# Kernel tuning notes

Hardware: AMD Instinct MI355X
Metric: run time of the kernel (lower is better)

## Reference

```python
import jax, jax.numpy as jnp
import numpy as np

H = 16  # num_heads
NEG = -1.0e9


def setup_inputs() -> dict:
    key = jax.random.key(0)
    ks = jax.random.split(key, 12)
    B, Q, D, S = 2, 2048, 1024, 512
    sc = 0.02
    return {
        "main_input": jax.random.normal(ks[0], (B, Q, D), jnp.float32),
        "side_input": jax.random.normal(ks[1], (S, D), jnp.float32),
        "att_mask": jax.random.randint(ks[2], (B, Q, Q + S), 0, 2, jnp.int32),
        "Wq": jax.random.normal(ks[3], (D, D), jnp.float32) * sc,
        "bq": jnp.zeros((D,), jnp.float32),
        "Wk": jax.random.normal(ks[4], (D, D), jnp.float32) * sc,
        "bk": jnp.zeros((D,), jnp.float32),
        "Wv": jax.random.normal(ks[5], (D, D), jnp.float32) * sc,
        "bv": jnp.zeros((D,), jnp.float32),
        "Wo": jax.random.normal(ks[6], (D, D), jnp.float32) * sc,
        "bo": jnp.zeros((D,), jnp.float32),
    }


def _heads(x, W, b):
    # x: [..., D] -> [..., H, d]
    y = x @ W + b
    return y.reshape(y.shape[:-1] + (H, y.shape[-1] // H))


def reference(main_input, side_input, att_mask, Wq, bq, Wk, bk, Wv, bv, Wo, bo):
    B, Q, D = main_input.shape
    S = side_input.shape[0]
    d = D // H
    q = _heads(main_input, Wq, bq)          # [B,Q,H,d]
    k = _heads(main_input, Wk, bk)          # [B,Q,H,d]
    v = _heads(main_input, Wv, bv)          # [B,Q,H,d]
    sk = _heads(side_input, Wk, bk)         # [S,H,d] (shared projections)
    sv = _heads(side_input, Wv, bv)         # [S,H,d]
    scores_main = jnp.einsum('bqhd,bkhd->bhqk', q, k)
    scores_side = jnp.einsum('bqhd,khd->bhqk', q, sk)
    scores = jnp.concatenate([scores_main, scores_side], axis=3)  # [B,H,Q,Q+S]
    scores = scores / jnp.sqrt(jnp.asarray(d, scores.dtype))
    adder = NEG * (1.0 - att_mask.astype(scores.dtype))[:, None, :, :]
    probs = jax.nn.softmax(scores + adder, axis=-1)
    out_main = jnp.einsum('bhqk,bkhd->bqhd', probs[..., :Q], v)
    out_side = jnp.einsum('bhqk,khd->bqhd', probs[..., Q:], sv)
    att = (out_main + out_side).reshape(B, Q, D)
    return att @ Wo + bo
```

## Files before the change

### kernel.cpp

```cpp
#include <hip/hip_runtime.h>
#include <cstdint>

typedef short s16x8 __attribute__((ext_vector_type(8)));
typedef short s16x4 __attribute__((ext_vector_type(4)));
typedef unsigned short u16x4 __attribute__((ext_vector_type(4)));
typedef float f32x4 __attribute__((ext_vector_type(4)));
typedef float f32x16 __attribute__((ext_vector_type(16)));
typedef unsigned int u32x4 __attribute__((ext_vector_type(4)));

#define ND 1024
#define NH 16
#define DH 64
#define NQ 2048
#define NL 2560
#define MMAIN 4096
#define MCAT 4608
#define Q_SCALE 0.18033688011112042f

__device__ __forceinline__ unsigned short f2b(float f) {
  unsigned u = __builtin_bit_cast(unsigned, f);
  u += 0x7FFFu + ((u >> 16) & 1u);
  return (unsigned short)(u >> 16);
}

__device__ __forceinline__ void gload16(const void* g, void* l) {
  __builtin_amdgcn_global_load_lds(
      (const __attribute__((address_space(1))) void*)(unsigned long long)(uintptr_t)g,
      (__attribute__((address_space(3))) void*)(unsigned)(uintptr_t)l,
      16, 0, 0);
}

__device__ __forceinline__ f32x4 mfma16(s16x8 a, s16x8 b, f32x4 c) {
  return __builtin_amdgcn_mfma_f32_16x16x32_bf16(a, b, c, 0, 0, 0);
}
__device__ __forceinline__ f32x16 mfma32(s16x8 a, s16x8 b, f32x16 c) {
  return __builtin_amdgcn_mfma_f32_32x32x16_bf16(a, b, c, 0, 0, 0);
}

__device__ __forceinline__ float exp2g(float x) {
#if __has_builtin(__builtin_amdgcn_exp2f)
  return __builtin_amdgcn_exp2f(x);
#else
  return exp2f(x);
#endif
}

__device__ __forceinline__ int sext_bit(unsigned w, int c) {
#if __has_builtin(__builtin_amdgcn_sbfe)
  return __builtin_amdgcn_sbfe((int)w, c, 1);
#else
  return -(int)((w >> c) & 1u);
#endif
}

__device__ __forceinline__ unsigned cvt_pk_bf16(float lo, float hi) {
  unsigned d;
  asm("v_cvt_pk_bf16_f32 %0, %1, %2" : "=v"(d) : "v"(lo), "v"(hi));
  return d;
}

__device__ __forceinline__ void plane32_swap(unsigned& a, unsigned& b) {
  asm("v_permlane32_swap_b32 %0, %1" : "+v"(a), "+v"(b));
}

__device__ __forceinline__ f32x16 z16() {
  f32x16 v;
#pragma unroll
  for (int i = 0; i < 16; ++i) v[i] = 0.f;
  return v;
}


__global__ __launch_bounds__(256) void k_convert_x(const float* __restrict__ mainp,
                                                   const float* __restrict__ sidep,
                                                   short* __restrict__ xcat) {
  size_t i4 = ((size_t)blockIdx.x * 256 + threadIdx.x) * 4;
  const float* src = (i4 < (size_t)MMAIN * ND) ? (mainp + i4) : (sidep + (i4 - (size_t)MMAIN * ND));
  float4 v = *(const float4*)src;
  s16x4 o;
  o[0] = (short)f2b(v.x); o[1] = (short)f2b(v.y);
  o[2] = (short)f2b(v.z); o[3] = (short)f2b(v.w);
  *(s16x4*)(xcat + i4) = o;
}

__global__ __launch_bounds__(256) void k_transpose_w(const float* __restrict__ W0,
                                                     const float* __restrict__ W1,
                                                     const float* __restrict__ W2,
                                                     const float* __restrict__ W3,
                                                     short* __restrict__ Wt) {
  __shared__ float T[64][65];
  const float* W = blockIdx.z == 0 ? W0 : blockIdx.z == 1 ? W1 : blockIdx.z == 2 ? W2 : W3;
  short* out = Wt + (size_t)blockIdx.z * (ND * ND);
  const int tid = threadIdx.x;
  const int r = tid >> 2, c0 = (tid & 3) * 16;
  const int k0 = blockIdx.x * 64, n0 = blockIdx.y * 64;
#pragma unroll
  for (int i = 0; i < 4; ++i) {
    float4 v = *(const float4*)(W + (size_t)(k0 + r) * ND + n0 + c0 + i * 4);
    T[r][c0 + i * 4 + 0] = v.x; T[r][c0 + i * 4 + 1] = v.y;
    T[r][c0 + i * 4 + 2] = v.z; T[r][c0 + i * 4 + 3] = v.w;
  }
  __syncthreads();
  s16x8 o0, o1;
#pragma unroll
  for (int i = 0; i < 8; ++i) o0[i] = (short)f2b(T[c0 + i][r]);
#pragma unroll
  for (int i = 0; i < 8; ++i) o1[i] = (short)f2b(T[c0 + 8 + i][r]);
  *(s16x8*)(out + (size_t)(n0 + r) * ND + k0 + c0) = o0;
  *(s16x8*)(out + (size_t)(n0 + r) * ND + k0 + c0 + 8) = o1;
}

__global__ __launch_bounds__(256) void k_pack_mask(const int* __restrict__ mask,
                                                   unsigned* __restrict__ pm) {
  int W = blockIdx.x * 256 + threadIdx.x;
  const int4* src = (const int4*)(mask + (size_t)W * 32);
  unsigned bits = 0;
#pragma unroll
  for (int i = 0; i < 8; ++i) {
    int4 v = src[i];
    bits |= (unsigned)(v.x & 1) << (i * 4 + 0);
    bits |= (unsigned)(v.y & 1) << (i * 4 + 1);
    bits |= (unsigned)(v.z & 1) << (i * 4 + 2);
    bits |= (unsigned)(v.w & 1) << (i * 4 + 3);
  }
  pm[W] = bits;
}


__global__ __launch_bounds__(256) void k_gemm_qkv(const short* __restrict__ A,
                                                  const short* __restrict__ Bt,
                                                  const float* __restrict__ bqp,
                                                  const float* __restrict__ bkp,
                                                  const float* __restrict__ bvp,
                                                  short* __restrict__ qb,
                                                  short* __restrict__ kb,
                                                  short* __restrict__ vt) {
  __shared__ __align__(16) short As[128 * 64];
  __shared__ __align__(16) short Bs[128 * 64];
  const int tid = threadIdx.x;
  const int w = tid >> 6, l = tid & 63;
  const int lg = l >> 4, li = l & 15;
  const int wr = w >> 1, wc = w & 1;
  const int fid = blockIdx.x + 24 * blockIdx.y;
  const int rid = (fid & 7) * 108 + (fid >> 3);
  const int m0 = (rid / 24) * 128, n0 = (rid % 24) * 128;

  f32x4 acc[4][4];
#pragma unroll
  for (int i = 0; i < 4; ++i)
#pragma unroll
    for (int j = 0; j < 4; ++j) acc[i][j] = (f32x4){0.f, 0.f, 0.f, 0.f};

  const int cb = (l & 7) ^ (l >> 3);
  const int rsub = l >> 3;

  for (int kt = 0; kt < 16; ++kt) {
    __syncthreads();
#pragma unroll
    for (int i = 0; i < 4; ++i) {
      int c = w * 4 + i;
      int rr = c * 8 + rsub;
      gload16(A + (size_t)(m0 + rr) * ND + kt * 64 + cb * 8, As + c * 512);
      gload16(Bt + (size_t)(n0 + rr) * ND + kt * 64 + cb * 8, Bs + c * 512);
    }
    __syncthreads();
#pragma unroll
    for (int kk = 0; kk < 2; ++kk) {
      const int blk = (((kk * 4) + lg) ^ (l & 7)) * 8;
      s16x8 af[4], bf[4];
#pragma unroll
      for (int mf = 0; mf < 4; ++mf)
        af[mf] = *(const s16x8*)(As + (wr * 64 + mf * 16 + li) * 64 + blk);
#pragma unroll
      for (int nf = 0; nf < 4; ++nf)
        bf[nf] = *(const s16x8*)(Bs + (wc * 64 + nf * 16 + li) * 64 + blk);
#pragma unroll
      for (int mf = 0; mf < 4; ++mf)
#pragma unroll
        for (int nf = 0; nf < 4; ++nf)
          acc[mf][nf] = mfma16(af[mf], bf[nf], acc[mf][nf]);
    }
  }

#pragma unroll
  for (int mf = 0; mf < 4; ++mf) {
#pragma unroll
    for (int nf = 0; nf < 4; ++nf) {
      const int n = n0 + wc * 64 + nf * 16 + li;
      const int proj = n >> 10, nn = n & 1023;
      const int h = nn >> 6, dd = nn & 63;
      const float bn = (proj == 0 ? bqp : proj == 1 ? bkp : bvp)[nn];
      const int mbase = m0 + wr * 64 + mf * 16 + lg * 4;
      if (proj == 0) {
        if (mbase < MMAIN) {
#pragma unroll
          for (int r = 0; r < 4; ++r) {
            int m = mbase + r;
            int b = m >> 11, q = m & 2047;
            qb[((size_t)(b * NH + h) * NQ + q) * DH + dd] =
                (short)f2b((acc[mf][nf][r] + bn) * Q_SCALE);
          }
        }
      } else if (proj == 1) {
#pragma unroll
        for (int r = 0; r < 4; ++r) {
          int m = mbase + r;
          short v = (short)f2b(acc[mf][nf][r] + bn);
          if (m < MMAIN) {
            int b = m >> 11, p = m & 2047;
            kb[((size_t)(b * NH + h) * NL + p) * DH + dd] = v;
          } else {
            int p = NQ + (m - MMAIN);
            kb[((size_t)h * NL + p) * DH + dd] = v;
            kb[((size_t)(NH + h) * NL + p) * DH + dd] = v;
          }
        }
      } else {
        u16x4 vv;
#pragma unroll
        for (int r = 0; r < 4; ++r) vv[r] = f2b(acc[mf][nf][r] + bn);
        if (mbase < MMAIN) {
          int b = mbase >> 11, p = mbase & 2047;
          *(u16x4*)(vt + ((size_t)(b * NH + h) * DH + dd) * NL + p) = vv;
        } else {
          int p = NQ + (mbase - MMAIN);
          *(u16x4*)(vt + ((size_t)h * DH + dd) * NL + p) = vv;
          *(u16x4*)(vt + ((size_t)(NH + h) * DH + dd) * NL + p) = vv;
        }
      }
    }
  }
}


__global__ __launch_bounds__(256) void k_gemm_out(const short* __restrict__ A,
                                                  const short* __restrict__ Bt,
                                                  const float* __restrict__ bias,
                                                  float* __restrict__ outp) {
  __shared__ __align__(16) short As[128 * 64];
  __shared__ __align__(16) short Bs[128 * 64];
  const int tid = threadIdx.x;
  const int w = tid >> 6, l = tid & 63;
  const int lg = l >> 4, li = l & 15;
  const int wr = w >> 1, wc = w & 1;
  const int fid = blockIdx.x + 8 * blockIdx.y;
  const int rid = (fid & 7) * 32 + (fid >> 3);
  const int m0 = (rid / 8) * 128, n0 = (rid % 8) * 128;

  f32x4 acc[4][4];
#pragma unroll
  for (int i = 0; i < 4; ++i)
#pragma unroll
    for (int j = 0; j < 4; ++j) acc[i][j] = (f32x4){0.f, 0.f, 0.f, 0.f};

  const int cb = (l & 7) ^ (l >> 3);
  const int rsub = l >> 3;

  for (int kt = 0; kt < 16; ++kt) {
    __syncthreads();
#pragma unroll
    for (int i = 0; i < 4; ++i) {
      int c = w * 4 + i;
      int rr = c * 8 + rsub;
      gload16(A + (size_t)(m0 + rr) * ND + kt * 64 + cb * 8, As + c * 512);
      gload16(Bt + (size_t)(n0 + rr) * ND + kt * 64 + cb * 8, Bs + c * 512);
    }
    __syncthreads();
#pragma unroll
    for (int kk = 0; kk < 2; ++kk) {
      const int blk = (((kk * 4) + lg) ^ (l & 7)) * 8;
      s16x8 af[4], bf[4];
#pragma unroll
      for (int mf = 0; mf < 4; ++mf)
        af[mf] = *(const s16x8*)(As + (wr * 64 + mf * 16 + li) * 64 + blk);
#pragma unroll
      for (int nf = 0; nf < 4; ++nf)
        bf[nf] = *(const s16x8*)(Bs + (wc * 64 + nf * 16 + li) * 64 + blk);
#pragma unroll
      for (int mf = 0; mf < 4; ++mf)
#pragma unroll
        for (int nf = 0; nf < 4; ++nf)
          acc[mf][nf] = mfma16(af[mf], bf[nf], acc[mf][nf]);
    }
  }

#pragma unroll
  for (int mf = 0; mf < 4; ++mf) {
#pragma unroll
    for (int nf = 0; nf < 4; ++nf) {
      const int n = n0 + wc * 64 + nf * 16 + li;
      const float bn = bias[n];
      const int mbase = m0 + wr * 64 + mf * 16 + lg * 4;
#pragma unroll
      for (int r = 0; r < 4; ++r)
        outp[(size_t)(mbase + r) * ND + n] = acc[mf][nf][r] + bn;
    }
  }
}


#define PROC_TILE(STV, WSV, PB0, PB1)                                        \
  do {                                                                       \
    unsigned pk_[8];                                                         \
    _Pragma("unroll") for (int r_ = 0; r_ < 16; ++r_) {                      \
      const int c_ = (r_ & 3) + 8 * (r_ >> 2);                               \
      float p_ = exp2g(STV[r_]);                                             \
      STV[r_] = __builtin_bit_cast(                                          \
          float, __builtin_bit_cast(unsigned, p_) &                          \
                     (unsigned)sext_bit(WSV, c_));                           \
    }                                                                        \
    _Pragma("unroll") for (int m_ = 0; m_ < 8; ++m_)                         \
        pk_[m_] = cvt_pk_bf16(STV[2 * m_], STV[2 * m_ + 1]);                 \
    plane32_swap(pk_[0], pk_[2]);                                            \
    plane32_swap(pk_[1], pk_[3]);                                            \
    plane32_swap(pk_[4], pk_[6]);                                            \
    plane32_swap(pk_[5], pk_[7]);                                            \
    {                                                                        \
      u32x4 t_ = {pk_[0], pk_[1], pk_[2], pk_[3]};                           \
      PB0 = __builtin_bit_cast(s16x8, t_);                                   \
    }                                                                        \
    {                                                                        \
      u32x4 t_ = {pk_[4], pk_[5], pk_[6], pk_[7]};                           \
      PB1 = __builtin_bit_cast(s16x8, t_);                                   \
    }                                                                        \
  } while (0)

#define ATTN_TILE(CUR, T, DONEXT)                                            \
  do {                                                                       \
    uint2 mw_ = *(const uint2*)(pmrow + 2 * (T));                            \
    if (DONEXT) {                                                            \
      const int tn_ = (T) + 1;                                               \
      gload16(kg0 + (size_t)tn_ * 4096, klA + ((CUR) ^ 1) * 8192);           \
      gload16(kg1 + (size_t)tn_ * 4096, klB + ((CUR) ^ 1) * 8192);           \
      gload16(vg0 + tn_ * 64, vlA + ((CUR) ^ 1) * 8192);                     \
      gload16(vg1 + tn_ * 64, vlB + ((CUR) ^ 1) * 8192);                     \
    }                                                                        \
    f32x16 st0_, st1_;                                                       \
    __builtin_amdgcn_s_setprio(1);                                           \
    {                                                                        \
      s16x8 k0_ = *(const s16x8*)(ldsb + (CUR) * 8192 + koff[0]);            \
      s16x8 k1_ = *(const s16x8*)(ldsb + (CUR) * 8192 + koff[0] + 4096);     \
      st0_ = mfma32(k0_, qa[0], ZACC);                                       \
      st1_ = mfma32(k1_, qa[0], ZACC);                                       \
    }                                                                        \
    _Pragma("unroll") for (int ks_ = 1; ks_ < 4; ++ks_) {                    \
      s16x8 k0_ = *(const s16x8*)(ldsb + (CUR) * 8192 + koff[ks_]);          \
      s16x8 k1_ = *(const s16x8*)(ldsb + (CUR) * 8192 + koff[ks_] + 4096);   \
      st0_ = mfma32(k0_, qa[ks_], st0_);                                     \
      st1_ = mfma32(k1_, qa[ks_], st1_);                                     \
    }                                                                        \
    __builtin_amdgcn_s_setprio(0);                                           \
    unsigned ws0_ = mw_.x >> (hi * 4), ws1_ = mw_.y >> (hi * 4);             \
    s16x8 pbA_[4];                                                           \
    PROC_TILE(st0_, ws0_, pbA_[0], pbA_[1]);                                 \
    PROC_TILE(st1_, ws1_, pbA_[2], pbA_[3]);                                 \
    __builtin_amdgcn_s_setprio(1);                                           \
    _Pragma("unroll") for (int ks_ = 0; ks_ < 4; ++ks_) {                    \
      s16x8 v0_ = *(const s16x8*)(ldsb + 16384 + (CUR) * 8192 + koff[ks_]);  \
      s16x8 v1_ =                                                            \
          *(const s16x8*)(ldsb + 16384 + (CUR) * 8192 + koff[ks_] + 4096);   \
      ot0 = mfma32(v0_, pbA_[ks_], ot0);                                     \
      ot1 = mfma32(v1_, pbA_[ks_], ot1);                                     \
      lacc = mfma32(ones8, pbA_[ks_], lacc);                                 \
    }                                                                        \
    __builtin_amdgcn_s_setprio(0);                                           \
    __syncthreads();                                                         \
  } while (0)

__global__ __launch_bounds__(256) void k_attn2(const short* __restrict__ qbuf,
                                               const short* __restrict__ kbuf,
                                               const short* __restrict__ vtbuf,
                                               const unsigned* __restrict__ pmask,
                                               short* __restrict__ attbuf) {
  __shared__ __align__(16) short lds[16384];
  char* ldsb = (char*)lds;

  const int tid = threadIdx.x;
  const int w = tid >> 6, l = tid & 63;
  const int li = l & 31, hi = l >> 5;
  const int bh = blockIdx.x;
  const int b = bh >> 4, h = bh & 15;
  const int qr0 = blockIdx.y * 128 + w * 32;
  const size_t bhs = (size_t)bh;

  s16x8 qa[4];
  {
    const short* qp = qbuf + (bhs * NQ + qr0 + li) * DH + hi * 8;
#pragma unroll
    for (int ks = 0; ks < 4; ++ks) qa[ks] = *(const s16x8*)(qp + ks * 16);
  }

  int koff[4];
#pragma unroll
  for (int ks = 0; ks < 4; ++ks)
    koff[ks] = li * 128 + ((((ks << 1) | hi) ^ (li & 7)) << 4);

  const int crow = l >> 3;
  const int ccol = (l & 7) ^ crow;
  const short* kg0 = kbuf + (bhs * NL + (2 * w) * 8 + crow) * DH + ccol * 8;
  const short* kg1 = kbuf + (bhs * NL + (2 * w + 1) * 8 + crow) * DH + ccol * 8;
  const short* vg0 = vtbuf + (bhs * DH + (2 * w) * 8 + crow) * NL + ccol * 8;
  const short* vg1 = vtbuf + (bhs * DH + (2 * w + 1) * 8 + crow) * NL + ccol * 8;
  char* klA = ldsb + (2 * w) * 1024;
  char* klB = ldsb + (2 * w + 1) * 1024;
  char* vlA = ldsb + 16384 + (2 * w) * 1024;
  char* vlB = ldsb + 16384 + (2 * w + 1) * 1024;

  const unsigned* pmrow = pmask + ((size_t)b * NQ + qr0 + li) * 80;

  const f32x16 ZACC = z16();
  f32x16 ot0 = z16(), ot1 = z16(), lacc = z16();
  s16x8 ones8;
#pragma unroll
  for (int i = 0; i < 8; ++i) ones8[i] = (short)0x3F80;

  gload16(kg0, klA);
  gload16(kg1, klB);
  gload16(vg0, vlA);
  gload16(vg1, vlB);
  __syncthreads();

  for (int tt = 0; tt < 20; ++tt) {
    const int t0 = 2 * tt;
    ATTN_TILE(0, t0, 1);
    ATTN_TILE(1, t0 + 1, (t0 + 2 < 40));
  }

  const float inv = 1.0f / lacc[0];
  short* orow = attbuf + ((size_t)b * NQ + qr0 + li) * ND + h * 64;
#pragma unroll
  for (int g = 0; g < 4; ++g) {
    u16x4 v0, v1;
#pragma unroll
    for (int r = 0; r < 4; ++r) {
      v0[r] = f2b(ot0[g * 4 + r] * inv);
      v1[r] = f2b(ot1[g * 4 + r] * inv);
    }
    *(u16x4*)(orow + g * 8 + hi * 4) = v0;
    *(u16x4*)(orow + 32 + g * 8 + hi * 4) = v1;
  }
}


extern "C" void kernel_launch(void* const* d_in, const int* in_sizes, int n_in,
                              void* d_out, int out_size, void* d_ws, size_t ws_size,
                              hipStream_t stream) {
  const float* mainp = (const float*)d_in[0];
  const float* sidep = (const float*)d_in[1];
  const int* mask = (const int*)d_in[2];
  const float* Wq = (const float*)d_in[3];
  const float* bq = (const float*)d_in[4];
  const float* Wk = (const float*)d_in[5];
  const float* bk = (const float*)d_in[6];
  const float* Wv = (const float*)d_in[7];
  const float* bv = (const float*)d_in[8];
  const float* Wo = (const float*)d_in[9];
  const float* bo = (const float*)d_in[10];

  char* ws = (char*)d_ws;
  short* xcat   = (short*)(ws + 0);
  short* Wt     = (short*)(ws + 9437184);
  short* qbuf   = (short*)(ws + 17825792);
  short* kbuf   = (short*)(ws + 26214400);
  short* vtbuf  = (short*)(ws + 36700160);
  short* attbuf = (short*)(ws + 47185920);
  unsigned* pmask = (unsigned*)(ws + 55574528);

  k_convert_x<<<4608, 256, 0, stream>>>(mainp, sidep, xcat);
  k_transpose_w<<<dim3(16, 16, 4), 256, 0, stream>>>(Wq, Wk, Wv, Wo, Wt);
  k_pack_mask<<<1280, 256, 0, stream>>>(mask, pmask);

  k_gemm_qkv<<<dim3(24, 36), 256, 0, stream>>>(xcat, Wt, bq, bk, bv, qbuf, kbuf, vtbuf);

  k_attn2<<<dim3(32, 16), 256, 0, stream>>>(qbuf, kbuf, vtbuf, pmask, attbuf);

  k_gemm_out<<<dim3(8, 32), 256, 0, stream>>>(attbuf, Wt + 3145728, bo, (float*)d_out);
}
```

Measured before the change: 161.7 us.

## Split attention KV range across two wave groups and combine via LDS

The attention block grows to 512 threads. Two groups of four waves each process half of the 2560 keys for the same query rows, with separate LDS double buffers. Afterwards the second group writes its partial output and row sum to LDS, and the first group adds them, normalizes and stores. This halves the serial key loop per wave and raises occupancy, at the cost of double the LDS use, an extra combine barrier, and a tighter register budget from __launch_bounds__(512,4) that could cause spills.

Measured after the change: 215.0 us. +33.0%, slower.

```diff
diff --git a/kernel.cpp b/kernel.cpp
--- a/kernel.cpp
+++ b/kernel.cpp
@@ -338,14 +338,14 @@
     f32x16 st0_, st1_;                                                       \
     __builtin_amdgcn_s_setprio(1);                                           \
     {                                                                        \
-      s16x8 k0_ = *(const s16x8*)(ldsb + (CUR) * 8192 + koff[0]);            \
-      s16x8 k1_ = *(const s16x8*)(ldsb + (CUR) * 8192 + koff[0] + 4096);     \
+      s16x8 k0_ = *(const s16x8*)(ldsg + (CUR) * 8192 + koff[0]);            \
+      s16x8 k1_ = *(const s16x8*)(ldsg + (CUR) * 8192 + koff[0] + 4096);     \
       st0_ = mfma32(k0_, qa[0], ZACC);                                       \
       st1_ = mfma32(k1_, qa[0], ZACC);                                       \
     }                                                                        \
     _Pragma("unroll") for (int ks_ = 1; ks_ < 4; ++ks_) {                    \
-      s16x8 k0_ = *(const s16x8*)(ldsb + (CUR) * 8192 + koff[ks_]);          \
-      s16x8 k1_ = *(const s16x8*)(ldsb + (CUR) * 8192 + koff[ks_] + 4096);   \
+      s16x8 k0_ = *(const s16x8*)(ldsg + (CUR) * 8192 + koff[ks_]);          \
+      s16x8 k1_ = *(const s16x8*)(ldsg + (CUR) * 8192 + koff[ks_] + 4096);   \
       st0_ = mfma32(k0_, qa[ks_], st0_);                                     \
       st1_ = mfma32(k1_, qa[ks_], st1_);                                     \
     }                                                                        \
@@ -356,9 +356,9 @@
     PROC_TILE(st1_, ws1_, pbA_[2], pbA_[3]);                                 \
     __builtin_amdgcn_s_setprio(1);                                           \
     _Pragma("unroll") for (int ks_ = 0; ks_ < 4; ++ks_) {                    \
-      s16x8 v0_ = *(const s16x8*)(ldsb + 16384 + (CUR) * 8192 + koff[ks_]);  \
+      s16x8 v0_ = *(const s16x8*)(ldsg + 16384 + (CUR) * 8192 + koff[ks_]);  \
       s16x8 v1_ =                                                            \
-          *(const s16x8*)(ldsb + 16384 + (CUR) * 8192 + koff[ks_] + 4096);   \
+          *(const s16x8*)(ldsg + 16384 + (CUR) * 8192 + koff[ks_] + 4096);   \
       ot0 = mfma32(v0_, pbA_[ks_], ot0);                                     \
       ot1 = mfma32(v1_, pbA_[ks_], ot1);                                     \
       lacc = mfma32(ones8, pbA_[ks_], lacc);                                 \
@@ -367,21 +367,23 @@
     __syncthreads();                                                         \
   } while (0)
 
-__global__ __launch_bounds__(256) void k_attn2(const short* __restrict__ qbuf,
-                                               const short* __restrict__ kbuf,
-                                               const short* __restrict__ vtbuf,
-                                               const unsigned* __restrict__ pmask,
-                                               short* __restrict__ attbuf) {
-  __shared__ __align__(16) short lds[16384];
+__global__ __launch_bounds__(512, 4) void k_attn2(const short* __restrict__ qbuf,
+                                                  const short* __restrict__ kbuf,
+                                                  const short* __restrict__ vtbuf,
+                                                  const unsigned* __restrict__ pmask,
+                                                  short* __restrict__ attbuf) {
+  __shared__ __align__(16) short lds[32768];
   char* ldsb = (char*)lds;
 
   const int tid = threadIdx.x;
   const int w = tid >> 6, l = tid & 63;
+  const int wg = w & 3, g = w >> 2;
   const int li = l & 31, hi = l >> 5;
   const int bh = blockIdx.x;
   const int b = bh >> 4, h = bh & 15;
-  const int qr0 = blockIdx.y * 128 + w * 32;
+  const int qr0 = blockIdx.y * 128 + wg * 32;
   const size_t bhs = (size_t)bh;
+  char* ldsg = ldsb + g * 32768;
 
   s16x8 qa[4];
   {
@@ -397,16 +399,16 @@
 
   const int crow = l >> 3;
   const int ccol = (l & 7) ^ crow;
-  const short* kg0 = kbuf + (bhs * NL + (2 * w) * 8 + crow) * DH + ccol * 8;
-  const short* kg1 = kbuf + (bhs * NL + (2 * w + 1) * 8 + crow) * DH + ccol * 8;
-  const short* vg0 = vtbuf + (bhs * DH + (2 * w) * 8 + crow) * NL + ccol * 8;
-  const short* vg1 = vtbuf + (bhs * DH + (2 * w + 1) * 8 + crow) * NL + ccol * 8;
-  char* klA = ldsb + (2 * w) * 1024;
-  char* klB = ldsb + (2 * w + 1) * 1024;
-  char* vlA = ldsb + 16384 + (2 * w) * 1024;
-  char* vlB = ldsb + 16384 + (2 * w + 1) * 1024;
-
-  const unsigned* pmrow = pmask + ((size_t)b * NQ + qr0 + li) * 80;
+  const short* kg0 = kbuf + (bhs * NL + g * 1280 + (2 * wg) * 8 + crow) * DH + ccol * 8;
+  const short* kg1 = kbuf + (bhs * NL + g * 1280 + (2 * wg + 1) * 8 + crow) * DH + ccol * 8;
+  const short* vg0 = vtbuf + (bhs * DH + (2 * wg) * 8 + crow) * NL + g * 1280 + ccol * 8;
+  const short* vg1 = vtbuf + (bhs * DH + (2 * wg + 1) * 8 + crow) * NL + g * 1280 + ccol * 8;
+  char* klA = ldsg + (2 * wg) * 1024;
+  char* klB = ldsg + (2 * wg + 1) * 1024;
+  char* vlA = ldsg + 16384 + (2 * wg) * 1024;
+  char* vlB = ldsg + 16384 + (2 * wg + 1) * 1024;
+
+  const unsigned* pmrow = pmask + ((size_t)b * NQ + qr0 + li) * 80 + g * 40;
 
   const f32x16 ZACC = z16();
   f32x16 ot0 = z16(), ot1 = z16(), lacc = z16();
@@ -420,24 +422,40 @@
   gload16(vg1, vlB);
   __syncthreads();
 
-  for (int tt = 0; tt < 20; ++tt) {
+  for (int tt = 0; tt < 10; ++tt) {
     const int t0 = 2 * tt;
     ATTN_TILE(0, t0, 1);
-    ATTN_TILE(1, t0 + 1, (t0 + 2 < 40));
-  }
-
-  const float inv = 1.0f / lacc[0];
-  short* orow = attbuf + ((size_t)b * NQ + qr0 + li) * ND + h * 64;
-#pragma unroll
-  for (int g = 0; g < 4; ++g) {
-    u16x4 v0, v1;
-#pragma unroll
-    for (int r = 0; r < 4; ++r) {
-      v0[r] = f2b(ot0[g * 4 + r] * inv);
-      v1[r] = f2b(ot1[g * 4 + r] * inv);
-    }
-    *(u16x4*)(orow + g * 8 + hi * 4) = v0;
-    *(u16x4*)(orow + 32 + g * 8 + hi * 4) = v1;
+    ATTN_TILE(1, t0 + 1, (t0 + 2 < 20));
+  }
+
+  float* comb = (float*)ldsb;
+  const int slot = (wg * 64 + l) * 33;
+  if (g == 1) {
+#pragma unroll
+    for (int i = 0; i < 16; ++i) comb[slot + i] = ot0[i];
+#pragma unroll
+    for (int i = 0; i < 16; ++i) comb[slot + 16 + i] = ot1[i];
+    comb[slot + 32] = lacc[0];
+  }
+  __syncthreads();
+  if (g == 0) {
+#pragma unroll
+    for (int i = 0; i < 16; ++i) ot0[i] += comb[slot + i];
+#pragma unroll
+    for (int i = 0; i < 16; ++i) ot1[i] += comb[slot + 16 + i];
+    const float inv = 1.0f / (lacc[0] + comb[slot + 32]);
+    short* orow = attbuf + ((size_t)b * NQ + qr0 + li) * ND + h * 64;
+#pragma unroll
+    for (int gg = 0; gg < 4; ++gg) {
+      u16x4 v0, v1;
+#pragma unroll
+      for (int r = 0; r < 4; ++r) {
+        v0[r] = f2b(ot0[gg * 4 + r] * inv);
+        v1[r] = f2b(ot1[gg * 4 + r] * inv);
+      }
+      *(u16x4*)(orow + gg * 8 + hi * 4) = v0;
+      *(u16x4*)(orow + 32 + gg * 8 + hi * 4) = v1;
+    }
   }
 }
 
@@ -472,7 +490,7 @@
 
   k_gemm_qkv<<<dim3(24, 36), 256, 0, stream>>>(xcat, Wt, bq, bk, bv, qbuf, kbuf, vtbuf);
 
-  k_attn2<<<dim3(32, 16), 256, 0, stream>>>(qbuf, kbuf, vtbuf, pmask, attbuf);
+  k_attn2<<<dim3(32, 16), 512, 0, stream>>>(qbuf, kbuf, vtbuf, pmask, attbuf);
 
   k_gemm_out<<<dim3(8, 32), 256, 0, stream>>>(attbuf, Wt + 3145728, bo, (float*)d_out);
 }
```
